# Kernel tuning notes

Measured on AMD Instinct MI355X. Metric: run time of the kernel, lower is better.

The kernel has to match this reference:

```python
import jax, jax.numpy as jnp
import numpy as np

TEMPERATURE = 0.5
EPS = 1e-8  # torch CosineSimilarity eps
NEG_INF = -1e9


def setup_inputs() -> dict:
    key = jax.random.key(0)
    k1, k2 = jax.random.split(key)
    B, D = 4096, 256
    return {
        "z_i": jax.random.normal(k1, (B, D), dtype=jnp.float32),
        "z_j": jax.random.normal(k2, (B, D), dtype=jnp.float32),
    }


def reference(z_i, z_j):
    B = z_i.shape[0]
    N = 2 * B
    z = jnp.concatenate([z_i, z_j], axis=0)  # [N, D]
    # Cosine similarity = GEMM of L2-normalized rows (same math as broadcasted CosineSimilarity)
    zn = z / jnp.maximum(jnp.linalg.norm(z, axis=1, keepdims=True), EPS)
    sim = (zn @ zn.T) / TEMPERATURE  # [N, N]
    # Positives: the (i, i+B) and (i+B, i) off-diagonals
    pos = jnp.concatenate([jnp.diagonal(sim, B), jnp.diagonal(sim, -B)])  # [N]
    # CE with label 0 over logits = [positive, negatives...]. The logit set per row
    # equals the sim row minus its self-diagonal entry (positive appears exactly once).
    sim_masked = jnp.where(jnp.eye(N, dtype=bool), NEG_INF, sim)
    lse = jax.nn.logsumexp(sim_masked, axis=1)  # [N]
    # CrossEntropyLoss(reduction='sum') / N == mean over rows
    return jnp.mean(lse - pos)
```

## Files before the change

### kernel.cpp

```cpp
#include <hip/hip_runtime.h>
#include <hip/hip_bf16.h>

#define NN 8192
#define BB 4096
#define DD 256
#define TILE 128
#define NT 64
#define NBLK 2080
#define KSCALE 2.8853900817779268f

typedef __attribute__((ext_vector_type(8))) short short8;
typedef __attribute__((ext_vector_type(4))) float f32x4;

static __device__ __forceinline__ float exp2_fast(float x) {
    float r; asm("v_exp_f32 %0, %1" : "=v"(r) : "v"(x)); return r;
}
static __device__ __forceinline__ ushort f2bf(float x) {
    __hip_bfloat16 h = __float2bfloat16(x);
    return *reinterpret_cast<ushort*>(&h);
}
static __device__ __forceinline__ float bf2f(short u) {
    unsigned int x = (unsigned int)(ushort)u << 16;
    float f; __builtin_memcpy(&f, &x, 4); return f;
}

__global__ __launch_bounds__(256) void norm_kernel(const float* __restrict__ zi,
                                                   const float* __restrict__ zj,
                                                   ushort* __restrict__ zn,
                                                   ushort* __restrict__ zns,
                                                   float* __restrict__ out) {
    if (blockIdx.x == 0 && threadIdx.x == 0) out[0] = 0.f;
    int row  = (blockIdx.x * 256 + threadIdx.x) >> 6;
    int lane = threadIdx.x & 63;
    const float* src = (row < BB) ? (zi + (size_t)row * DD)
                                  : (zj + (size_t)(row - BB) * DD);
    float4 v = ((const float4*)src)[lane];
    float ss = v.x * v.x + v.y * v.y + v.z * v.z + v.w * v.w;
    #pragma unroll
    for (int m = 32; m; m >>= 1) ss += __shfl_xor(ss, m, 64);
    float inv = 1.0f / fmaxf(sqrtf(ss), 1e-8f);
    ushort4 o, os;
    o.x  = f2bf(v.x * inv);            o.y  = f2bf(v.y * inv);
    o.z  = f2bf(v.z * inv);            o.w  = f2bf(v.w * inv);
    float invs = inv * KSCALE;
    os.x = f2bf(v.x * invs);           os.y = f2bf(v.y * invs);
    os.z = f2bf(v.z * invs);           os.w = f2bf(v.w * invs);
    ((ushort4*)(zn  + (size_t)row * DD))[lane] = o;
    ((ushort4*)(zns + (size_t)row * DD))[lane] = os;
}

__global__ __launch_bounds__(128, 2) void sim_kernel(const ushort* __restrict__ zn,
                                                     const ushort* __restrict__ zns,
                                                     float* __restrict__ psum) {
    __shared__ int4  lds4[4][1024];
    __shared__ float csumW[2][TILE];

    const int tid  = threadIdx.x;
    const int w    = tid >> 6;
    const int lane = tid & 63;
    const int l15  = lane & 15;
    const int lhi  = lane >> 4;

    int bid = blockIdx.x;
    int idx = (bid & 7) * (NBLK / 8) + (bid >> 3);
    int bj  = (int)((sqrtf(8.0f * (float)idx + 1.0f) - 1.0f) * 0.5f);
    while ((bj + 1) * (bj + 2) / 2 <= idx) ++bj;
    while (bj * (bj + 1) / 2 > idx) --bj;
    int bi = idx - bj * (bj + 1) / 2;

    const int  rowbase = bi * TILE + w * 64;
    const int  colbase = bj * TILE;
    const bool offdiag = (bi != bj);

    short8 a[4][8];
    #pragma unroll
    for (int rt = 0; rt < 4; ++rt)
        #pragma unroll
        for (int kk = 0; kk < 8; ++kk)
            a[rt][kk] = *(const short8*)(zns + (size_t)(rowbase + rt * 16 + l15) * DD
                                             + kk * 32 + lhi * 8);

    #pragma unroll
    for (int ct = 0; ct < 4; ++ct)
        #pragma unroll
        for (int i = 0; i < 8; ++i) {
            int d = i * 128 + tid;
            int r = d >> 5, c = d & 31;
            const ushort* src = zn + (size_t)(colbase + ct * 32 + r) * DD
                                   + (size_t)((c ^ (r & 7)) * 8);
            __builtin_amdgcn_global_load_lds(
                (__attribute__((address_space(1))) void*)src,
                (__attribute__((address_space(3))) void*)&lds4[ct][i * 128 + w * 64],
                16, 0, 0);
        }
    __builtin_amdgcn_sched_barrier(0);

    f32x4 sume[4];
    #pragma unroll
    for (int rt = 0; rt < 4; ++rt) sume[rt] = (f32x4){0.f, 0.f, 0.f, 0.f};

    #pragma unroll
    for (int ct = 0; ct < 4; ++ct) {
        if      (ct == 0) asm volatile("s_waitcnt vmcnt(24)" ::: "memory");
        else if (ct == 1) asm volatile("s_waitcnt vmcnt(16)" ::: "memory");
        else if (ct == 2) asm volatile("s_waitcnt vmcnt(8)"  ::: "memory");
        else              asm volatile("s_waitcnt vmcnt(0)"  ::: "memory");
        __builtin_amdgcn_s_barrier();
        __builtin_amdgcn_sched_barrier(0);

        const short8* buf = (const short8*)lds4[ct];
        #pragma unroll
        for (int sub = 0; sub < 2; ++sub) {
            const int brow = sub * 16 + l15;
            short8 b[8];
            #pragma unroll
            for (int kk = 0; kk < 8; ++kk)
                b[kk] = buf[brow * 32 + ((kk * 4 + lhi) ^ (brow & 7))];
            f32x4 acc[4];
            #pragma unroll
            for (int rt = 0; rt < 4; ++rt) acc[rt] = (f32x4){0.f, 0.f, 0.f, 0.f};
            #pragma unroll
            for (int kk = 0; kk < 8; ++kk)
                #pragma unroll
                for (int rt = 0; rt < 4; ++rt)
                    acc[rt] = __builtin_amdgcn_mfma_f32_16x16x32_bf16(a[rt][kk], b[kk], acc[rt], 0, 0, 0);
            float cs = 0.f;
            #pragma unroll
            for (int rt = 0; rt < 4; ++rt)
                #pragma unroll
                for (int g = 0; g < 4; ++g) {
                    float e = exp2_fast(acc[rt][g]);
                    sume[rt][g] += e;
                    cs += e;
                }
            if (offdiag) {
                cs += __shfl_xor(cs, 16, 64);
                cs += __shfl_xor(cs, 32, 64);
                if (lhi == 0) csumW[w][ct * 32 + sub * 16 + l15] = cs;
            }
        }
    }

    #pragma unroll
    for (int rt = 0; rt < 4; ++rt)
        #pragma unroll
        for (int g = 0; g < 4; ++g) {
            float v = sume[rt][g];
            v += __shfl_xor(v, 1, 64); v += __shfl_xor(v, 2, 64);
            v += __shfl_xor(v, 4, 64); v += __shfl_xor(v, 8, 64);
            if (l15 == 0)
                psum[(size_t)bj * NN + rowbase + rt * 16 + lhi * 4 + g] = v;
        }
    if (offdiag) {
        __syncthreads();
        if (tid < TILE)
            psum[(size_t)bi * NN + colbase + tid] = csumW[0][tid] + csumW[1][tid];
    }
}

__global__ __launch_bounds__(1024) void reduce_kernel(const ushort* __restrict__ zn,
                                                      const ushort* __restrict__ zns,
                                                      const float* __restrict__ psum,
                                                      float* __restrict__ out) {
    const int tid  = threadIdx.x;
    const int rloc = tid >> 4;
    const int r    = blockIdx.x * 64 + rloc;
    const int l    = tid & 15;

    float S = 0.f;
    #pragma unroll
    for (int i = 0; i < 4; ++i) S += psum[(size_t)(i * 16 + l) * NN + r];

    const ushort* zr = zn  + (size_t)r * DD + l * 16;
    const ushort* sr = zns + (size_t)r * DD + l * 16;
    const ushort* pr = zn  + (size_t)(r ^ BB) * DD + l * 16;
    short8 z0 = *(const short8*)zr, z1 = *(const short8*)(zr + 8);
    short8 s0 = *(const short8*)sr, s1 = *(const short8*)(sr + 8);
    short8 p0 = *(const short8*)pr, p1 = *(const short8*)(pr + 8);
    float ds = 0.f, dp = 0.f;
    #pragma unroll
    for (int k = 0; k < 8; ++k) {
        float za = bf2f(z0[k]), zb = bf2f(z1[k]);
        ds += bf2f(s0[k]) * za + bf2f(s1[k]) * zb;
        dp += bf2f(p0[k]) * za + bf2f(p1[k]) * zb;
    }
    #pragma unroll
    for (int m = 1; m < 16; m <<= 1) {
        S  += __shfl_xor(S,  m, 64);
        ds += __shfl_xor(ds, m, 64);
        dp += __shfl_xor(dp, m, 64);
    }
    __shared__ float red[64];
    if (l == 0) red[rloc] = logf(S - exp2_fast(ds)) - 2.0f * dp;
    __syncthreads();
    if (tid < 64) {
        float v = red[tid];
        #pragma unroll
        for (int m = 32; m; m >>= 1) v += __shfl_xor(v, m, 64);
        if (tid == 0) atomicAdd(out, v * (1.0f / NN));
    }
}

extern "C" void kernel_launch(void* const* d_in, const int* in_sizes, int n_in,
                              void* d_out, int out_size, void* d_ws, size_t ws_size,
                              hipStream_t stream) {
    const float* zi = (const float*)d_in[0];
    const float* zj = (const float*)d_in[1];
    float* out = (float*)d_out;

    char* ws = (char*)d_ws;
    ushort* zn   = (ushort*)ws;
    ushort* zns  = (ushort*)(ws + (size_t)NN * DD * 2);
    float*  psum = (float*)(ws + (size_t)NN * DD * 4);

    norm_kernel<<<NN / 4, 256, 0, stream>>>(zi, zj, zn, zns, out);
    sim_kernel<<<NBLK, 128, 0, stream>>>(zn, zns, psum);
    reduce_kernel<<<NN / 64, 1024, 0, stream>>>(zn, zns, psum, out);
}
```

Baseline: 125.2 us.

## Restructure sim GEMM into 4-wave 2x2 tiling with double-buffered K-staged LDS

The sim kernel moves from 2 waves that each hold a 64-row A panel in registers and stream B from LDS to 4 waves in a 2x2 layout. A and B are both staged through double-buffered LDS in K-chunks of 32, with a 4x4 MFMA accumulator block per wave. This cuts register pressure and shares the A and B loads across waves, in exchange for a barrier per K step and a bigger accumulator set. The LDS layout drops the XOR swizzle, so bank conflicts may appear, and the exp and row/column sums now run only after the full K loop.

```diff
diff --git a/kernel.cpp b/kernel.cpp
--- a/kernel.cpp
+++ b/kernel.cpp
@@ -49,17 +49,21 @@
     ((ushort4*)(zns + (size_t)row * DD))[lane] = os;
 }
 
-__global__ __launch_bounds__(128, 2) void sim_kernel(const ushort* __restrict__ zn,
-                                                     const ushort* __restrict__ zns,
-                                                     float* __restrict__ psum) {
-    __shared__ int4  lds4[4][1024];
-    __shared__ float csumW[2][TILE];
+__global__ __launch_bounds__(256) void sim_kernel(const ushort* __restrict__ zn,
+                                                  const ushort* __restrict__ zns,
+                                                  float* __restrict__ psum) {
+    __shared__ int4  ldsA[2][512];
+    __shared__ int4  ldsB[2][512];
+    __shared__ float rsumL[2][2][64];
+    __shared__ float csumL[2][2][64];
 
     const int tid  = threadIdx.x;
     const int w    = tid >> 6;
     const int lane = tid & 63;
     const int l15  = lane & 15;
     const int lhi  = lane >> 4;
+    const int wr   = w >> 1;
+    const int wc   = w & 1;
 
     int bid = blockIdx.x;
     int idx = (bid & 7) * (NBLK / 8) + (bid >> 3);
@@ -68,94 +72,100 @@
     while (bj * (bj + 1) / 2 > idx) --bj;
     int bi = idx - bj * (bj + 1) / 2;
 
-    const int  rowbase = bi * TILE + w * 64;
-    const int  colbase = bj * TILE;
+    const int  rowt0   = bi * TILE;
+    const int  colt0   = bj * TILE;
     const bool offdiag = (bi != bj);
 
-    short8 a[4][8];
-    #pragma unroll
-    for (int rt = 0; rt < 4; ++rt)
-        #pragma unroll
-        for (int kk = 0; kk < 8; ++kk)
-            a[rt][kk] = *(const short8*)(zns + (size_t)(rowbase + rt * 16 + l15) * DD
-                                             + kk * 32 + lhi * 8);
-
-    #pragma unroll
-    for (int ct = 0; ct < 4; ++ct)
-        #pragma unroll
-        for (int i = 0; i < 8; ++i) {
-            int d = i * 128 + tid;
-            int r = d >> 5, c = d & 31;
-            const ushort* src = zn + (size_t)(colbase + ct * 32 + r) * DD
-                                   + (size_t)((c ^ (r & 7)) * 8);
+    auto STAGE = [&](int buf, int k) {
+        #pragma unroll
+        for (int i = 0; i < 2; ++i) {
+            int d = i * 256 + tid;
+            int r = d >> 2, g = d & 3;
+            const ushort* sa = zns + (size_t)(rowt0 + r) * DD + k * 32 + g * 8;
             __builtin_amdgcn_global_load_lds(
-                (__attribute__((address_space(1))) void*)src,
-                (__attribute__((address_space(3))) void*)&lds4[ct][i * 128 + w * 64],
+                (__attribute__((address_space(1))) void*)sa,
+                (__attribute__((address_space(3))) void*)&ldsA[buf][i * 256 + w * 64],
+                16, 0, 0);
+            const ushort* sb = zn + (size_t)(colt0 + r) * DD + k * 32 + g * 8;
+            __builtin_amdgcn_global_load_lds(
+                (__attribute__((address_space(1))) void*)sb,
+                (__attribute__((address_space(3))) void*)&ldsB[buf][i * 256 + w * 64],
                 16, 0, 0);
         }
-    __builtin_amdgcn_sched_barrier(0);
-
-    f32x4 sume[4];
-    #pragma unroll
-    for (int rt = 0; rt < 4; ++rt) sume[rt] = (f32x4){0.f, 0.f, 0.f, 0.f};
-
-    #pragma unroll
-    for (int ct = 0; ct < 4; ++ct) {
-        if      (ct == 0) asm volatile("s_waitcnt vmcnt(24)" ::: "memory");
-        else if (ct == 1) asm volatile("s_waitcnt vmcnt(16)" ::: "memory");
-        else if (ct == 2) asm volatile("s_waitcnt vmcnt(8)"  ::: "memory");
-        else              asm volatile("s_waitcnt vmcnt(0)"  ::: "memory");
-        __builtin_amdgcn_s_barrier();
-        __builtin_amdgcn_sched_barrier(0);
-
-        const short8* buf = (const short8*)lds4[ct];
-        #pragma unroll
-        for (int sub = 0; sub < 2; ++sub) {
-            const int brow = sub * 16 + l15;
-            short8 b[8];
+    };
+
+    f32x4 acc[4][4];
+    #pragma unroll
+    for (int mi = 0; mi < 4; ++mi)
+        #pragma unroll
+        for (int ni = 0; ni < 4; ++ni) acc[mi][ni] = (f32x4){0.f, 0.f, 0.f, 0.f};
+
+    STAGE(0, 0);
+    __syncthreads();
+
+    #pragma unroll
+    for (int k = 0; k < 8; ++k) {
+        if (k < 7) STAGE((k + 1) & 1, k + 1);
+        const short8* bufA = (const short8*)ldsA[k & 1];
+        const short8* bufB = (const short8*)ldsB[k & 1];
+        short8 af[4], bfr[4];
+        #pragma unroll
+        for (int mi = 0; mi < 4; ++mi)
+            af[mi] = bufA[(wr * 64 + mi * 16 + l15) * 4 + lhi];
+        #pragma unroll
+        for (int ni = 0; ni < 4; ++ni)
+            bfr[ni] = bufB[(wc * 64 + ni * 16 + l15) * 4 + lhi];
+        #pragma unroll
+        for (int mi = 0; mi < 4; ++mi)
             #pragma unroll
-            for (int kk = 0; kk < 8; ++kk)
-                b[kk] = buf[brow * 32 + ((kk * 4 + lhi) ^ (brow & 7))];
-            f32x4 acc[4];
+            for (int ni = 0; ni < 4; ++ni)
+                acc[mi][ni] = __builtin_amdgcn_mfma_f32_16x16x32_bf16(af[mi], bfr[ni], acc[mi][ni], 0, 0, 0);
+        __syncthreads();
+    }
+
+    float rpart[4][4];
+    float cpart[4];
+    #pragma unroll
+    for (int mi = 0; mi < 4; ++mi)
+        #pragma unroll
+        for (int g = 0; g < 4; ++g) rpart[mi][g] = 0.f;
+    #pragma unroll
+    for (int ni = 0; ni < 4; ++ni) cpart[ni] = 0.f;
+
+    #pragma unroll
+    for (int mi = 0; mi < 4; ++mi)
+        #pragma unroll
+        for (int ni = 0; ni < 4; ++ni)
             #pragma unroll
-            for (int rt = 0; rt < 4; ++rt) acc[rt] = (f32x4){0.f, 0.f, 0.f, 0.f};
-            #pragma unroll
-            for (int kk = 0; kk < 8; ++kk)
-                #pragma unroll
-                for (int rt = 0; rt < 4; ++rt)
-                    acc[rt] = __builtin_amdgcn_mfma_f32_16x16x32_bf16(a[rt][kk], b[kk], acc[rt], 0, 0, 0);
-            float cs = 0.f;
-            #pragma unroll
-            for (int rt = 0; rt < 4; ++rt)
-                #pragma unroll
-                for (int g = 0; g < 4; ++g) {
-                    float e = exp2_fast(acc[rt][g]);
-                    sume[rt][g] += e;
-                    cs += e;
-                }
-            if (offdiag) {
-                cs += __shfl_xor(cs, 16, 64);
-                cs += __shfl_xor(cs, 32, 64);
-                if (lhi == 0) csumW[w][ct * 32 + sub * 16 + l15] = cs;
+            for (int g = 0; g < 4; ++g) {
+                float e = exp2_fast(acc[mi][ni][g]);
+                rpart[mi][g] += e;
+                cpart[ni]    += e;
             }
-        }
-    }
-
-    #pragma unroll
-    for (int rt = 0; rt < 4; ++rt)
+
+    #pragma unroll
+    for (int mi = 0; mi < 4; ++mi)
         #pragma unroll
         for (int g = 0; g < 4; ++g) {
-            float v = sume[rt][g];
+            float v = rpart[mi][g];
             v += __shfl_xor(v, 1, 64); v += __shfl_xor(v, 2, 64);
             v += __shfl_xor(v, 4, 64); v += __shfl_xor(v, 8, 64);
-            if (l15 == 0)
-                psum[(size_t)bj * NN + rowbase + rt * 16 + lhi * 4 + g] = v;
+            if (l15 == 0) rsumL[wr][wc][mi * 16 + lhi * 4 + g] = v;
         }
-    if (offdiag) {
-        __syncthreads();
-        if (tid < TILE)
-            psum[(size_t)bi * NN + colbase + tid] = csumW[0][tid] + csumW[1][tid];
-    }
+    #pragma unroll
+    for (int ni = 0; ni < 4; ++ni) {
+        float v = cpart[ni];
+        v += __shfl_xor(v, 16, 64); v += __shfl_xor(v, 32, 64);
+        if (lhi == 0) csumL[wc][wr][ni * 16 + l15] = v;
+    }
+    __syncthreads();
+
+    if (tid < TILE)
+        psum[(size_t)bj * NN + rowt0 + tid] =
+            rsumL[tid >> 6][0][tid & 63] + rsumL[tid >> 6][1][tid & 63];
+    if (offdiag && tid < TILE)
+        psum[(size_t)bi * NN + colt0 + tid] =
+            csumL[tid >> 6][0][tid & 63] + csumL[tid >> 6][1][tid & 63];
 }
 
 __global__ __launch_bounds__(1024) void reduce_kernel(const ushort* __restrict__ zn,
@@ -214,6 +224,6 @@
     float*  psum = (float*)(ws + (size_t)NN * DD * 4);
 
     norm_kernel<<<NN / 4, 256, 0, stream>>>(zi, zj, zn, zns, out);
-    sim_kernel<<<NBLK, 128, 0, stream>>>(zn, zns, psum);
+    sim_kernel<<<NBLK, 256, 0, stream>>>(zn, zns, psum);
     reduce_kernel<<<NN / 64, 1024, 0, stream>>>(zn, zns, psum, out);
 }
```

Measured after the change: 112.5 us. 1.11x faster.
